# Optimization experiments

Measured on AMD Instinct MI355X. Metric: run time of the kernel, lower is better.

Reference implementation:

```python
import jax, jax.numpy as jnp
import numpy as np

B, S, D_MODEL, N_HEADS, D_FF = 4, 2048, 1024, 16, 4096
HEAD_DIM = D_MODEL // N_HEADS
NUM_BUCKETS, MAX_DISTANCE = 32, 128
EPS = 1e-6


def _relative_position_bucket(relative_position, num_buckets=NUM_BUCKETS, max_distance=MAX_DISTANCE):
    # bidirectional (encoder) variant, matching T5RelativePositionBias
    n = -relative_position
    nb = num_buckets // 2
    ret = (n < 0).astype(jnp.int32) * nb
    n = jnp.abs(n)
    max_exact = nb // 2
    val_if_large = max_exact + (
        jnp.log(jnp.maximum(n, 1).astype(jnp.float32) / max_exact)
        / np.log(max_distance / max_exact) * (nb - max_exact)
    ).astype(jnp.int32)
    val_if_large = jnp.minimum(val_if_large, nb - 1)
    return ret + jnp.where(n < max_exact, n, val_if_large)


def t5_position_bias(rel_emb, q_len, k_len):
    ctx = jnp.arange(q_len)[:, None]
    mem = jnp.arange(k_len)[None, :]
    rp_bucket = _relative_position_bucket(mem - ctx)          # [S, S]
    bias = rel_emb[rp_bucket]                                  # [S, S, H]
    return jnp.transpose(bias, (2, 0, 1))[None]                # [1, H, S, S]


def layer_norm(x, g, b):
    mu = jnp.mean(x, axis=-1, keepdims=True)
    var = jnp.mean(jnp.square(x - mu), axis=-1, keepdims=True)
    return (x - mu) * jax.lax.rsqrt(var + EPS) * g + b


def setup_inputs() -> dict:
    key = jax.random.key(0)
    ks = jax.random.split(key, 20)
    s = 0.02
    p = {
        'src': jax.random.normal(ks[0], (B, S, D_MODEL), jnp.float32),
        'wq': jax.random.normal(ks[1], (D_MODEL, D_MODEL), jnp.float32) * s,
        'bq': jnp.zeros((D_MODEL,), jnp.float32),
        'wk': jax.random.normal(ks[2], (D_MODEL, D_MODEL), jnp.float32) * s,
        'bk': jnp.zeros((D_MODEL,), jnp.float32),
        'wv': jax.random.normal(ks[3], (D_MODEL, D_MODEL), jnp.float32) * s,
        'bv': jnp.zeros((D_MODEL,), jnp.float32),
        'wo': jax.random.normal(ks[4], (D_MODEL, D_MODEL), jnp.float32) * s,
        'bo': jnp.zeros((D_MODEL,), jnp.float32),
        'w1': jax.random.normal(ks[5], (D_MODEL, D_FF), jnp.float32) * s,
        'b1': jnp.zeros((D_FF,), jnp.float32),
        'w2': jax.random.normal(ks[6], (D_FF, D_MODEL), jnp.float32) * s,
        'b2': jnp.zeros((D_MODEL,), jnp.float32),
        'ln1_g': jnp.ones((D_MODEL,), jnp.float32),
        'ln1_b': jnp.zeros((D_MODEL,), jnp.float32),
        'ln2_g': jnp.ones((D_MODEL,), jnp.float32),
        'ln2_b': jnp.zeros((D_MODEL,), jnp.float32),
        'rel_emb': jax.random.normal(ks[7], (NUM_BUCKETS, N_HEADS), jnp.float32) * s,
    }
    return p


def reference(src, wq, bq, wk, bk, wv, bv, wo, bo, w1, b1, w2, b2,
              ln1_g, ln1_b, ln2_g, ln2_b, rel_emb):
    b, s, _ = src.shape

    # --- self-attention block (pre-norm) ---
    xn = layer_norm(src, ln1_g, ln1_b)
    q = (xn @ wq + bq).reshape(b, s, N_HEADS, HEAD_DIM).transpose(0, 2, 1, 3)
    k = (xn @ wk + bk).reshape(b, s, N_HEADS, HEAD_DIM).transpose(0, 2, 1, 3)
    v = (xn @ wv + bv).reshape(b, s, N_HEADS, HEAD_DIM).transpose(0, 2, 1, 3)

    bias = t5_position_bias(rel_emb, s, s)                       # [1,H,S,S]
    scores = jnp.einsum('bhqd,bhkd->bhqk', q, k) / np.sqrt(HEAD_DIM) + bias
    attn = jax.nn.softmax(scores, axis=-1)
    ctx = jnp.einsum('bhqk,bhkd->bhqd', attn, v)                 # [B,H,S,Dh]
    ctx = ctx.transpose(0, 2, 1, 3).reshape(b, s, D_MODEL)
    x = src + (ctx @ wo + bo)

    # --- FFN block (pre-norm, ReLU) ---
    yn = layer_norm(x, ln2_g, ln2_b)
    y = jax.nn.relu(yn @ w1 + b1) @ w2 + b2
    return x + y
```

## Files before the change

kernel.cpp:

```cpp
#include <hip/hip_runtime.h>
#include <math.h>

typedef unsigned short u16;

#define S_LEN 2048
#define BSZ 4
#define DM 1024
#define NH 16
#define HD 64
#define DFF 4096
#define ROWS (BSZ * S_LEN)
#define LOG2E 1.4426950408889634f

typedef __attribute__((__ext_vector_type__(8))) __bf16 bf16x8;
typedef __attribute__((__ext_vector_type__(8))) short short8;
typedef __attribute__((__ext_vector_type__(4))) short short4v;
typedef __attribute__((__ext_vector_type__(4))) float f32x4;
typedef __attribute__((__ext_vector_type__(4))) float float4v;

__device__ __forceinline__ float bf2f(u16 u) {
    union { unsigned int i; float f; } c; c.i = ((unsigned int)u) << 16; return c.f;
}
__device__ __forceinline__ u16 f2bf(float f) {
    union { float f; unsigned int i; } c; c.f = f;
    unsigned int r = c.i + 0x7fffu + ((c.i >> 16) & 1u);
    return (u16)(r >> 16);
}
__device__ __forceinline__ u16 f2bf_cvt(float f) {
    __bf16 h = (__bf16)f;
    return __builtin_bit_cast(u16, h);
}
__device__ __forceinline__ float ldin(const void* p, long i, int f32) {
    return f32 ? ((const float*)p)[i] : bf2f(((const u16*)p)[i]);
}
__device__ __forceinline__ int dtype_f32(const u16* ln1g) {
    return ln1g[0] != 0x3F80;
}
__device__ __forceinline__ void gl_lds16(const void* g, void* l) {
    __builtin_amdgcn_global_load_lds(
        (const __attribute__((address_space(1))) unsigned int*)g,
        (__attribute__((address_space(3))) unsigned int*)l, 16, 0, 0);
}

#define BARR  asm volatile("s_barrier" ::: "memory")
#define LGKM0 asm volatile("s_waitcnt lgkmcnt(0)" ::: "memory")
#define VM4   asm volatile("s_waitcnt vmcnt(4)" ::: "memory")
#define VM2   asm volatile("s_waitcnt vmcnt(2)" ::: "memory")
#define VM0   asm volatile("s_waitcnt vmcnt(0)" ::: "memory")

__device__ __forceinline__ void tr_tile(
    const void* __restrict__ src, u16* __restrict__ dst, int N, int K,
    int bx, int by, int f32, int tid, u16 (*t)[72])
{
#pragma unroll
    for (int i = 0; i < 2; i++) {
        int c = tid + i * 256;
        int row = c >> 3, col = (c & 7) * 8;
        long off = (long)(by * 64 + row) * N + bx * 64 + col;
        short8 v;
        if (f32) {
            const float* s = (const float*)src + off;
            float4v a = *(const float4v*)s;
            float4v b = *(const float4v*)(s + 4);
#pragma unroll
            for (int k = 0; k < 4; k++) { v[k] = (short)f2bf(a[k]); v[k + 4] = (short)f2bf(b[k]); }
        } else {
            v = *(const short8*)((const u16*)src + off);
        }
        *(short8*)(&t[row][col]) = v;
    }
    __syncthreads();
#pragma unroll
    for (int i = 0; i < 2; i++) {
        int c = tid + i * 256;
        int row = c >> 3, col = (c & 7) * 8;
        short8 v;
#pragma unroll
        for (int jj = 0; jj < 8; jj++) v[jj] = (short)t[col + jj][row];
        *(short8*)(dst + (long)(bx * 64 + row) * K + by * 64 + col) = v;
    }
}

__global__ __launch_bounds__(256) void transpose4(
    const void* wq, const void* wk, const void* wv, const void* wo,
    u16* __restrict__ wqkvt, u16* __restrict__ wot, const u16* __restrict__ ln1g)
{
    __shared__ u16 t[64][72];
    int z = blockIdx.z;
    const void* src = (z == 0) ? wq : (z == 1) ? wk : (z == 2) ? wv : wo;
    u16* dst = (z < 3) ? wqkvt + (long)z * 1024 * 1024 : wot;
    tr_tile(src, dst, DM, DM, blockIdx.x, blockIdx.y, dtype_f32(ln1g), threadIdx.x, t);
}

__global__ __launch_bounds__(256) void transpose2(
    const void* w1, const void* w2, u16* __restrict__ w1t, u16* __restrict__ w2t,
    const u16* __restrict__ ln1g)
{
    __shared__ u16 t[64][72];
    int f32 = dtype_f32(ln1g);
    if (blockIdx.z == 0)
        tr_tile(w1, w1t, DFF, DM, blockIdx.x, blockIdx.y, f32, threadIdx.x, t);
    else
        tr_tile(w2, w2t, DM, DFF, blockIdx.y, blockIdx.x, f32, threadIdx.x, t);
}

__global__ __launch_bounds__(256) void vtrans(
    const u16* __restrict__ v, u16* __restrict__ vt)
{
    __shared__ u16 t[64][72];
    int s0 = blockIdx.x * 64;
    int bh = blockIdx.y;
    const u16* src = v + (long)bh * S_LEN * HD;
    u16* dst = vt + (long)bh * HD * S_LEN;
    int tid = threadIdx.x;
#pragma unroll
    for (int i = 0; i < 2; i++) {
        int c = tid + i * 256;
        int row = c >> 3, col = (c & 7) * 8;
        *(short8*)(&t[row][col]) = *(const short8*)(src + (long)(s0 + row) * HD + col);
    }
    __syncthreads();
#pragma unroll
    for (int i = 0; i < 2; i++) {
        int c = tid + i * 256;
        int row = c >> 3, col = (c & 7) * 8;
        short8 o;
#pragma unroll
        for (int jj = 0; jj < 8; jj++) o[jj] = (short)t[col + jj][row];
        *(short8*)(dst + (long)row * S_LEN + s0 + col) = o;
    }
}

__global__ __launch_bounds__(256) void prep_kernel(
    const void* bq, const void* bk, const void* bv, const void* bo,
    const void* b1, const void* b2, const void* l1g, const void* l1b,
    const void* l2g, const void* l2b, const void* rel,
    u16* __restrict__ smalls, float* __restrict__ bias_full)
{
    int f32 = dtype_f32((const u16*)l1g);
    int tid = blockIdx.x * blockDim.x + threadIdx.x;
    if (tid < 13312) {
        float v;
        if      (tid < 1024)  v = ldin(bq,  tid,         f32);
        else if (tid < 2048)  v = ldin(bk,  tid - 1024,  f32);
        else if (tid < 3072)  v = ldin(bv,  tid - 2048,  f32);
        else if (tid < 4096)  v = ldin(bo,  tid - 3072,  f32);
        else if (tid < 8192)  v = ldin(b1,  tid - 4096,  f32);
        else if (tid < 9216)  v = ldin(b2,  tid - 8192,  f32);
        else if (tid < 10240) v = ldin(l1g, tid - 9216,  f32);
        else if (tid < 11264) v = ldin(l1b, tid - 10240, f32);
        else if (tid < 12288) v = ldin(l2g, tid - 11264, f32);
        else                  v = ldin(l2b, tid - 12288, f32);
        smalls[tid] = f2bf(v);
    }
    if (tid < 4095 * 16) {
        int dIdx = tid >> 4;
        int h = tid & 15;
        int delta = dIdx - 2047;
        int n = -delta;
        int ret = (n < 0) ? 16 : 0;
        int na = (n < 0) ? -n : n;
        int bkt;
        if (na < 8) {
            bkt = na;
        } else {
            float tval = logf((float)na * 0.125f) * 2.8853900817779268f;
            int v = 8 + (int)tval;
            bkt = v < 15 ? v : 15;
        }
        bkt += ret;
        bias_full[h * 4095 + dIdx] = ldin(rel, bkt * 16 + h, f32) * LOG2E;
    }
}

__global__ __launch_bounds__(256) void ln_kernel(
    const void* __restrict__ xin, int external, const u16* __restrict__ ln1g,
    const u16* __restrict__ g, const u16* __restrict__ bta, u16* __restrict__ out)
{
    int f32 = external ? dtype_f32(ln1g) : 0;
    int row = blockIdx.x;
    int tid = threadIdx.x;
    float vals[4];
    if (f32) {
        float4v v = *(const float4v*)((const float*)xin + (long)row * DM + tid * 4);
#pragma unroll
        for (int k = 0; k < 4; k++) vals[k] = v[k];
    } else {
        short4v v = *(const short4v*)((const u16*)xin + (long)row * DM + tid * 4);
#pragma unroll
        for (int k = 0; k < 4; k++) vals[k] = bf2f((u16)v[k]);
    }
    float s1 = 0.f, s2 = 0.f;
#pragma unroll
    for (int k = 0; k < 4; k++) { s1 += vals[k]; s2 += vals[k] * vals[k]; }
#pragma unroll
    for (int off = 32; off > 0; off >>= 1) {
        s1 += __shfl_xor(s1, off);
        s2 += __shfl_xor(s2, off);
    }
    __shared__ float ps1[4], ps2[4];
    int wave = tid >> 6, lane = tid & 63;
    if (lane == 0) { ps1[wave] = s1; ps2[wave] = s2; }
    __syncthreads();
    s1 = ps1[0] + ps1[1] + ps1[2] + ps1[3];
    s2 = ps2[0] + ps2[1] + ps2[2] + ps2[3];
    float mu = s1 * (1.0f / DM);
    float var = s2 * (1.0f / DM) - mu * mu;
    float rs = rsqrtf(var + 1e-6f);
    short4v ov;
#pragma unroll
    for (int k = 0; k < 4; k++) {
        float gv = bf2f(g[tid * 4 + k]);
        float bv = bf2f(bta[tid * 4 + k]);
        ov[k] = (short)f2bf((vals[k] - mu) * rs * gv + bv);
    }
    *(short4v*)(out + (long)row * DM + tid * 4) = ov;
}

#define TM 256
#define TN 256
#define TK 64

#define PHASE(bi, q, STAGE, WAITV)                                             \
    {                                                                          \
        if ((q) == 0) {                                                        \
            _Pragma("unroll")                                                  \
            for (int j = 0; j < 4; j++) {                                      \
                _Pragma("unroll")                                              \
                for (int t = 0; t < 2; t++)                                    \
                    bfr[j][t] = __builtin_bit_cast(bf16x8, *(const short8*)(   \
                        &Bs[bi][wn * 64 + j * 16 + l16][((t * 4 + quad) ^ rxor) * 8])); \
            }                                                                  \
        }                                                                      \
        _Pragma("unroll")                                                      \
        for (int i = 0; i < 2; i++) {                                          \
            _Pragma("unroll")                                                  \
            for (int t = 0; t < 2; t++)                                        \
                af[i][t] = __builtin_bit_cast(bf16x8, *(const short8*)(        \
                    &As[bi][wm * 128 + ((q) * 2 + i) * 16 + l16][((t * 4 + quad) ^ rxor) * 8])); \
        }                                                                      \
        STAGE                                                                  \
        WAITV;                                                                 \
        BARR;                                                                  \
        LGKM0;                                                                 \
        __builtin_amdgcn_sched_barrier(0);                                     \
        __builtin_amdgcn_s_setprio(1);                                         \
        _Pragma("unroll")                                                      \
        for (int i = 0; i < 2; i++) {                                          \
            _Pragma("unroll")                                                  \
            for (int j = 0; j < 4; j++) {                                      \
                acc[(q) * 2 + i][j] = __builtin_amdgcn_mfma_f32_16x16x32_bf16( \
                    af[i][0], bfr[j][0], acc[(q) * 2 + i][j], 0, 0, 0);        \
                acc[(q) * 2 + i][j] = __builtin_amdgcn_mfma_f32_16x16x32_bf16( \
                    af[i][1], bfr[j][1], acc[(q) * 2 + i][j], 0, 0, 0);        \
            }                                                                  \
        }                                                                      \
        __builtin_amdgcn_s_setprio(0);                                         \
        BARR;                                                                  \
    }

__global__ __launch_bounds__(512, 2) void gemm256(
    const u16* __restrict__ A, const u16* __restrict__ Bt,
    const u16* __restrict__ bias, int M, int N, int K, int mode,
    u16* __restrict__ out_q, u16* __restrict__ out_k, u16* __restrict__ out_v,
    u16* __restrict__ outp)
{
    __shared__ u16 As[2][TM][TK];
    __shared__ u16 Bs[2][TN][TK];

    int tid = threadIdx.x;
    int wavei = tid >> 6, lane = tid & 63;
    int quad = lane >> 4, l16 = lane & 15;
    int wm = wavei >> 2, wn = wavei & 3;

    int nwg = gridDim.x * gridDim.y;
    int bid = blockIdx.y * gridDim.x + blockIdx.x;
    int chunk = nwg >> 3;
    int swz = (bid & 7) * chunk + (bid >> 3);
    int bx = swz % gridDim.x, by = swz / gridDim.x;
    long m0 = (long)by * TM, n0 = (long)bx * TN;

    int srow = tid >> 3;
    int pchk = tid & 7;
    int cchk = pchk ^ (srow & 7);
    int rxor = l16 & 7;

    int NT = K / TK;

    auto stageA = [&](int bufi, int h, int t) {
        const u16* g = A + (m0 + h * 128 + srow) * (long)K + (long)t * TK + cchk * 8;
        gl_lds16(g,                 &As[bufi][h * 128 + srow     ][pchk * 8]);
        gl_lds16(g + 64 * (long)K,  &As[bufi][h * 128 + srow + 64][pchk * 8]);
    };
    auto stageB = [&](int bufi, int h, int t) {
        const u16* g = Bt + (n0 + h * 128 + srow) * (long)K + (long)t * TK + cchk * 8;
        gl_lds16(g,                 &Bs[bufi][h * 128 + srow     ][pchk * 8]);
        gl_lds16(g + 64 * (long)K,  &Bs[bufi][h * 128 + srow + 64][pchk * 8]);
    };

    f32x4 acc[8][4];
    f32x4 z = {0.f, 0.f, 0.f, 0.f};
#pragma unroll
    for (int i = 0; i < 8; i++)
#pragma unroll
        for (int j = 0; j < 4; j++) acc[i][j] = z;

    bf16x8 bfr[4][2];
    bf16x8 af[2][2];

    stageA(0, 0, 0); stageA(0, 1, 0); stageB(0, 0, 0); stageB(0, 1, 0);
    stageB(1, 0, 1); stageB(1, 1, 1);
    VM4;
    BARR;

    for (int kt = 0; kt < NT - 2; kt += 2) {
        PHASE(0, 0, { stageA(1, 0, kt + 1); stageA(1, 1, kt + 1); }, (void)0);
        PHASE(0, 1, { stageB(0, 0, kt + 2); }, (void)0);
        PHASE(0, 2, { stageB(0, 1, kt + 2); }, (void)0);
        PHASE(0, 3, {}, VM4);
        PHASE(1, 0, { stageA(0, 0, kt + 2); }, (void)0);
        PHASE(1, 1, { stageA(0, 1, kt + 2); stageB(1, 0, kt + 3); }, (void)0);
        PHASE(1, 2, { stageB(1, 1, kt + 3); }, (void)0);
        PHASE(1, 3, {}, VM4);
    }
    PHASE(0, 0, { stageA(1, 0, NT - 1); stageA(1, 1, NT - 1); }, (void)0);
    PHASE(0, 1, {}, (void)0);
    PHASE(0, 2, {}, (void)0);
    PHASE(0, 3, {}, VM0);
    PHASE(1, 0, {}, (void)0);
    PHASE(1, 1, {}, (void)0);
    PHASE(1, 2, {}, (void)0);
    PHASE(1, 3, {}, (void)0);

#pragma unroll
    for (int i = 0; i < 8; i++) {
#pragma unroll
        for (int j = 0; j < 4; j++) {
#pragma unroll
            for (int r = 0; r < 4; r++) {
                long gr = m0 + wm * 128 + i * 16 + quad * 4 + r;
                long gc = n0 + wn * 64 + j * 16 + l16;
                float val = acc[i][j][r] + bf2f(bias[gc]);
                if (mode == 1) {
                    int sel = (int)(gc >> 10);
                    int cc = (int)(gc & 1023);
                    int h = cc >> 6, d = cc & 63;
                    int b = (int)(gr >> 11), s = (int)(gr & 2047);
                    u16* dst = (sel == 0) ? out_q : (sel == 1 ? out_k : out_v);
                    dst[(((long)(b * NH + h)) * S_LEN + s) * HD + d] = f2bf(val);
                } else {
                    outp[gr * (long)N + gc] = f2bf(val > 0.f ? val : 0.f);
                }
            }
        }
    }
}

#define NBM 256
#define NBN 128

#define PHN(bi, half, STAGE, WAITV)                                            \
    {                                                                          \
        if ((half) == 0) {                                                     \
            _Pragma("unroll")                                                  \
            for (int j = 0; j < 2; j++) {                                      \
                _Pragma("unroll")                                              \
                for (int t = 0; t < 2; t++)                                    \
                    nbfr[j][t] = __builtin_bit_cast(bf16x8, *(const short8*)(  \
                        &Bs[bi][wn * 32 + j * 16 + l16][((t * 4 + quad) ^ rxor) * 8])); \
            }                                                                  \
        }                                                                      \
        _Pragma("unroll")                                                      \
        for (int i = 0; i < 4; i++) {                                          \
            _Pragma("unroll")                                                  \
            for (int t = 0; t < 2; t++)                                        \
                naf[i][t] = __builtin_bit_cast(bf16x8, *(const short8*)(       \
                    &As[bi][wm * 128 + ((half) * 4 + i) * 16 + l16][((t * 4 + quad) ^ rxor) * 8])); \
        }                                                                      \
        STAGE                                                                  \
        WAITV;                                                                 \
        BARR;                                                                  \
        LGKM0;                                                                 \
        __builtin_amdgcn_sched_barrier(0);                                     \
        __builtin_amdgcn_s_setprio(1);                                         \
        _Pragma("unroll")                                                      \
        for (int i = 0; i < 4; i++) {                                          \
            _Pragma("unroll")                                                  \
            for (int j = 0; j < 2; j++) {                                      \
                acc[(half) * 4 + i][j] = __builtin_amdgcn_mfma_f32_16x16x32_bf16( \
                    naf[i][0], nbfr[j][0], acc[(half) * 4 + i][j], 0, 0, 0);   \
                acc[(half) * 4 + i][j] = __builtin_amdgcn_mfma_f32_16x16x32_bf16( \
                    naf[i][1], nbfr[j][1], acc[(half) * 4 + i][j], 0, 0, 0);   \
            }                                                                  \
        }                                                                      \
        __builtin_amdgcn_s_setprio(0);                                         \
        BARR;                                                                  \
    }

__global__ __launch_bounds__(512, 2) void gemm256n(
    const u16* __restrict__ A, const u16* __restrict__ Bt,
    const u16* __restrict__ bias, int M, int N, int K, int mode,
    const void* __restrict__ res, void* __restrict__ outp,
    const u16* __restrict__ ln1g)
{
    __shared__ u16 As[2][NBM][TK];
    __shared__ u16 Bs[2][NBN][TK];

    int tid = threadIdx.x;
    int wavei = tid >> 6, lane = tid & 63;
    int quad = lane >> 4, l16 = lane & 15;
    int wm = wavei >> 2, wn = wavei & 3;

    int nwg = gridDim.x * gridDim.y;
    int bid = blockIdx.y * gridDim.x + blockIdx.x;
    int chunk = nwg >> 3;
    int swz = (bid & 7) * chunk + (bid >> 3);
    int bx = swz % gridDim.x, by = swz / gridDim.x;
    long m0 = (long)by * NBM, n0 = (long)bx * NBN;
    int flg = dtype_f32(ln1g);

    int srow = tid >> 3;
    int pchk = tid & 7;
    int cchk = pchk ^ (srow & 7);
    int rxor = l16 & 7;

    int NT = K / TK;

    auto stageA = [&](int bufi, int h, int t) {
        const u16* g = A + (m0 + h * 128 + srow) * (long)K + (long)t * TK + cchk * 8;
        gl_lds16(g,                 &As[bufi][h * 128 + srow     ][pchk * 8]);
        gl_lds16(g + 64 * (long)K,  &As[bufi][h * 128 + srow + 64][pchk * 8]);
    };
    auto stageB = [&](int bufi, int t) {
        const u16* g = Bt + (n0 + srow) * (long)K + (long)t * TK + cchk * 8;
        gl_lds16(g,                 &Bs[bufi][srow     ][pchk * 8]);
        gl_lds16(g + 64 * (long)K,  &Bs[bufi][srow + 64][pchk * 8]);
    };

    f32x4 acc[8][2];
    f32x4 z = {0.f, 0.f, 0.f, 0.f};
#pragma unroll
    for (int i = 0; i < 8; i++)
#pragma unroll
        for (int j = 0; j < 2; j++) acc[i][j] = z;

    bf16x8 nbfr[2][2];
    bf16x8 naf[4][2];

    stageA(0, 0, 0); stageA(0, 1, 0); stageB(0, 0);
    stageB(1, 1);
    VM2;
    BARR;

    for (int kt = 0; kt < NT - 2; kt += 2) {
        PHN(0, 0, { stageA(1, 0, kt + 1); stageA(1, 1, kt + 1); }, (void)0);
        PHN(0, 1, { stageB(0, kt + 2); }, VM2);
        PHN(1, 0, { stageA(0, 0, kt + 2); stageA(0, 1, kt + 2); }, (void)0);
        PHN(1, 1, { stageB(1, kt + 3); }, VM2);
    }
    PHN(0, 0, { stageA(1, 0, NT - 1); stageA(1, 1, NT - 1); }, (void)0);
    PHN(0, 1, {}, VM0);
    PHN(1, 0, {}, (void)0);
    PHN(1, 1, {}, (void)0);

#pragma unroll
    for (int i = 0; i < 8; i++) {
#pragma unroll
        for (int j = 0; j < 2; j++) {
#pragma unroll
            for (int r = 0; r < 4; r++) {
                long gr = m0 + wm * 128 + i * 16 + quad * 4 + r;
                long gc = n0 + wn * 32 + j * 16 + l16;
                float val = acc[i][j][r] + bf2f(bias[gc]);
                long idx = gr * (long)N + gc;
                if (mode == 2) {
                    float rv = flg ? ((const float*)res)[idx]
                                   : bf2f(((const u16*)res)[idx]);
                    ((u16*)outp)[idx] = f2bf(val + rv);
                } else {
                    float o = val + bf2f(((const u16*)res)[idx]);
                    if (flg) ((float*)outp)[idx] = o;
                    else     ((u16*)outp)[idx]  = f2bf(o);
                }
            }
        }
    }
}

__global__ __launch_bounds__(512, 4) void attn_kernel(
    const u16* __restrict__ Qg, const u16* __restrict__ Kg, const u16* __restrict__ Vtg,
    const float* __restrict__ bias_full, u16* __restrict__ ctx)
{
    __shared__ u16 Ks[64][64];
    __shared__ u16 Vt[64][64];
    __shared__ u16 Ps[128][72];
    __shared__ u16 bias_s[2176];

    int bh = blockIdx.y;
    int b = bh >> 4, h = bh & 15;
    int q0 = blockIdx.x * 128;
    const u16* Q  = Qg  + (long)bh * S_LEN * HD;
    const u16* Kp = Kg  + (long)bh * S_LEN * HD;
    const u16* Vp = Vtg + (long)bh * HD * S_LEN;

    int tid = threadIdx.x;
    int wave = tid >> 6, lane = tid & 63;
    int quad = lane >> 4, l16 = lane & 15;

    for (int i = tid; i < 2176; i += 512)
        bias_s[i] = f2bf(bias_full[h * 4095 + 1920 + i - q0]);
    float Bneg = bias_full[h * 4095 + 0];
    float Bpos = bias_full[h * 4095 + 4094];

    int isv = wave >= 4;
    int t2 = tid & 255;
    int prow = t2 >> 3, pchk = t2 & 7;
    int cchk = pchk ^ (prow & 7);
    int rxor = l16 & 7;
    int rc0 = (quad ^ rxor) * 8;
    int rc1 = ((4 + quad) ^ rxor) * 8;

    bf16x8 aq[2];
#pragma unroll
    for (int t = 0; t < 2; t++)
        aq[t] = __builtin_bit_cast(bf16x8,
            *(const short8*)(Q + (long)(q0 + wave * 16 + l16) * HD + t * 32 + quad * 8));

    bf16x8 ones;
#pragma unroll
    for (int i = 0; i < 8; i++) ones[i] = (__bf16)1.0f;

    f32x4 o[4];
    f32x4 z = {0.f, 0.f, 0.f, 0.f};
#pragma unroll
    for (int j = 0; j < 4; j++) o[j] = z;
    f32x4 lacc = z;

    int ib = 127 + quad * 4 - wave * 16 - l16;
    const float c0 = 0.125f * LOG2E;

    auto compute = [&](int t0) {
        f32x4 s_[4];
#pragma unroll
        for (int j = 0; j < 4; j++) {
            f32x4 a = z;
            bf16x8 kf0 = __builtin_bit_cast(bf16x8, *(const short8*)(&Ks[j * 16 + l16][rc0]));
            a = __builtin_amdgcn_mfma_f32_16x16x32_bf16(kf0, aq[0], a, 0, 0, 0);
            bf16x8 kf1 = __builtin_bit_cast(bf16x8, *(const short8*)(&Ks[j * 16 + l16][rc1]));
            a = __builtin_amdgcn_mfma_f32_16x16x32_bf16(kf1, aq[1], a, 0, 0, 0);
            s_[j] = a;
        }
        int d0 = t0 - q0;
        int nearb = (d0 >= -153 && d0 <= 217);
        float bconst = (d0 > 0) ? Bpos : Bneg;
#pragma unroll
        for (int j = 0; j < 4; j++) {
            short4v pk;
#pragma unroll
            for (int r = 0; r < 4; r++) {
                float bl = nearb ? bf2f(bias_s[ib + t0 + j * 16 + r]) : bconst;
                float p = __builtin_amdgcn_exp2f(fmaf(s_[j][r], c0, bl));
                pk[r] = (short)f2bf_cvt(p);
            }
            *(short4v*)(&Ps[wave * 16 + l16][j * 16 + quad * 4]) = pk;
        }
        bf16x8 ap[2];
#pragma unroll
        for (int tt = 0; tt < 2; tt++)
            ap[tt] = __builtin_bit_cast(bf16x8,
                *(const short8*)(&Ps[wave * 16 + l16][tt * 32 + quad * 8]));
        lacc = __builtin_amdgcn_mfma_f32_16x16x32_bf16(ap[0], ones, lacc, 0, 0, 0);
        lacc = __builtin_amdgcn_mfma_f32_16x16x32_bf16(ap[1], ones, lacc, 0, 0, 0);
#pragma unroll
        for (int j = 0; j < 4; j++) {
            f32x4 t = o[j];
            bf16x8 bv0 = __builtin_bit_cast(bf16x8, *(const short8*)(&Vt[j * 16 + l16][rc0]));
            t = __builtin_amdgcn_mfma_f32_16x16x32_bf16(ap[0], bv0, t, 0, 0, 0);
            bf16x8 bv1 = __builtin_bit_cast(bf16x8, *(const short8*)(&Vt[j * 16 + l16][rc1]));
            t = __builtin_amdgcn_mfma_f32_16x16x32_bf16(ap[1], bv1, t, 0, 0, 0);
            o[j] = t;
        }
    };

    auto ld0 = [&](int t) -> short8 {
        return isv ? *(const short8*)(Vp + (long)prow * S_LEN + t + cchk * 8)
                   : *(const short8*)(Kp + (long)(t + prow) * HD + cchk * 8);
    };
    auto ld1 = [&](int t) -> short8 {
        return isv ? *(const short8*)(Vp + (long)(32 + prow) * S_LEN + t + cchk * 8)
                   : *(const short8*)(Kp + (long)(t + 32 + prow) * HD + cchk * 8);
    };
    u16* dst0 = isv ? &Vt[prow][pchk * 8] : &Ks[prow][pchk * 8];
    u16* dst1 = isv ? &Vt[32 + prow][pchk * 8] : &Ks[32 + prow][pchk * 8];

    short8 sa0 = ld0(0), sa1 = ld1(0);
    short8 sb0, sb1;

    for (int t0 = 0; t0 < S_LEN; t0 += 128) {
        if (t0 > 0) BARR;
        VM0;
        *(short8*)dst0 = sa0;
        *(short8*)dst1 = sa1;
        sb0 = ld0(t0 + 64);
        sb1 = ld1(t0 + 64);
        LGKM0; BARR;
        compute(t0);

        BARR;
        VM0;
        *(short8*)dst0 = sb0;
        *(short8*)dst1 = sb1;
        if (t0 + 128 < S_LEN) {
            sa0 = ld0(t0 + 128);
            sa1 = ld1(t0 + 128);
        }
        LGKM0; BARR;
        compute(t0 + 64);
    }

#pragma unroll
    for (int r = 0; r < 4; r++) {
        int qr = wave * 16 + quad * 4 + r;
        float linv = 1.0f / lacc[r];
        long srow2 = (long)(b * S_LEN + q0 + qr);
#pragma unroll
        for (int j = 0; j < 4; j++)
            ctx[srow2 * DM + h * HD + j * 16 + l16] = f2bf(o[j][r] * linv);
    }
}

extern "C" void kernel_launch(void* const* d_in, const int* in_sizes, int n_in,
                              void* d_out, int out_size, void* d_ws, size_t ws_size,
                              hipStream_t stream)
{
    const void* src  = d_in[0];
    const void* wq   = d_in[1];
    const void* bq   = d_in[2];
    const void* wk   = d_in[3];
    const void* bk   = d_in[4];
    const void* wv   = d_in[5];
    const void* bv   = d_in[6];
    const void* wo   = d_in[7];
    const void* bo   = d_in[8];
    const void* w1   = d_in[9];
    const void* b1   = d_in[10];
    const void* w2   = d_in[11];
    const void* b2   = d_in[12];
    const void* ln1g = d_in[13];
    const void* ln1b = d_in[14];
    const void* ln2g = d_in[15];
    const void* ln2b = d_in[16];
    const void* rel  = d_in[17];
    const u16* l1g16 = (const u16*)ln1g;

    char* ws = (char*)d_ws;
    const long MB = 1L << 20;
    u16*   smalls = (u16*)  (ws);
    float* bfull  = (float*)(ws + 65536);
    u16*   xn     = (u16*)  (ws + 1  * MB);
    u16*   vtg    = (u16*)  (ws + 1  * MB);
    u16*   qws    = (u16*)  (ws + 17 * MB);
    u16*   kws    = (u16*)  (ws + 33 * MB);
    u16*   vws    = (u16*)  (ws + 49 * MB);
    u16*   hbuf   = (u16*)  (ws + 1  * MB);
    u16*   ctx    = (u16*)  (ws + 65 * MB);
    u16*   yn     = (u16*)  (ws + 65 * MB);
    u16*   xbf    = (u16*)  (ws + 81 * MB);
    u16*   wqkvt  = (u16*)  (ws + 97 * MB);
    u16*   wot    = (u16*)  (ws + 103 * MB);
    u16*   w1t    = (u16*)  (ws + 97 * MB);
    u16*   w2t    = (u16*)  (ws + 105 * MB);

    transpose4<<<dim3(16, 16, 4), 256, 0, stream>>>(wq, wk, wv, wo, wqkvt, wot, l1g16);
    prep_kernel<<<256, 256, 0, stream>>>(bq, bk, bv, bo, b1, b2,
                                         ln1g, ln1b, ln2g, ln2b, rel,
                                         smalls, bfull);

    ln_kernel<<<ROWS, 256, 0, stream>>>(src, 1, l1g16,
                                        smalls + 9216, smalls + 10240, xn);

    gemm256<<<dim3(3072 / TN, ROWS / TM), 512, 0, stream>>>(
        xn, wqkvt, smalls + 0, ROWS, 3072, DM, 1, qws, kws, vws, nullptr);

    vtrans<<<dim3(S_LEN / 64, BSZ * NH), 256, 0, stream>>>(vws, vtg);

    attn_kernel<<<dim3(S_LEN / 128, BSZ * NH), 512, 0, stream>>>(qws, kws, vtg, bfull, ctx);

    gemm256n<<<dim3(DM / NBN, ROWS / NBM), 512, 0, stream>>>(
        ctx, wot, smalls + 3072, ROWS, DM, DM, 2, src, xbf, l1g16);

    transpose2<<<dim3(64, 16, 2), 256, 0, stream>>>(w1, w2, w1t, w2t, l1g16);

    ln_kernel<<<ROWS, 256, 0, stream>>>(xbf, 0, l1g16,
                                        smalls + 11264, smalls + 12288, yn);

    gemm256<<<dim3(DFF / TN, ROWS / TM), 512, 0, stream>>>(
        yn, w1t, smalls + 4096, ROWS, DFF, DM, 3, nullptr, nullptr, nullptr, hbuf);

    gemm256n<<<dim3(DM / NBN, ROWS / NBM), 512, 0, stream>>>(
        hbuf, w2t, smalls + 8192, ROWS, DM, DFF, 4, xbf, d_out, l1g16);
}
```

Measured before the change: 569.6 us.

## Merge weight transposes and prep into one launch; swizzle attention blocks

Combines the four-weight transpose, the FFN weight transpose and the bias/params prep into a single prep_all launch with a z-indexed grid, moving w1t/w2t to separate workspace regions so they are no longer overwritten. The attention kernel remaps block IDs with an XCD-style swizzle so consecutive blocks on one XCD share the same head's K/V in cache. It also pads the Ps shared tile row from 72 to 76 to change bank mapping. Launch count drops, but the merged grid has many early-exit idle blocks, and the padding change may alter LDS conflicts either way.

```diff
diff --git a/kernel.cpp b/kernel.cpp
--- a/kernel.cpp
+++ b/kernel.cpp
@@ -81,64 +81,38 @@
     }
 }
 
-__global__ __launch_bounds__(256) void transpose4(
+__global__ __launch_bounds__(256) void prep_all(
     const void* wq, const void* wk, const void* wv, const void* wo,
-    u16* __restrict__ wqkvt, u16* __restrict__ wot, const u16* __restrict__ ln1g)
+    const void* w1, const void* w2,
+    const void* bq, const void* bk, const void* bv, const void* bo,
+    const void* b1, const void* b2, const void* l1g, const void* l1b,
+    const void* l2g, const void* l2b, const void* rel,
+    u16* __restrict__ wqkvt, u16* __restrict__ wot,
+    u16* __restrict__ w1t, u16* __restrict__ w2t,
+    u16* __restrict__ smalls, float* __restrict__ bias_full)
 {
     __shared__ u16 t[64][72];
     int z = blockIdx.z;
-    const void* src = (z == 0) ? wq : (z == 1) ? wk : (z == 2) ? wv : wo;
-    u16* dst = (z < 3) ? wqkvt + (long)z * 1024 * 1024 : wot;
-    tr_tile(src, dst, DM, DM, blockIdx.x, blockIdx.y, dtype_f32(ln1g), threadIdx.x, t);
-}
-
-__global__ __launch_bounds__(256) void transpose2(
-    const void* w1, const void* w2, u16* __restrict__ w1t, u16* __restrict__ w2t,
-    const u16* __restrict__ ln1g)
-{
-    __shared__ u16 t[64][72];
-    int f32 = dtype_f32(ln1g);
-    if (blockIdx.z == 0)
+    int f32 = dtype_f32((const u16*)l1g);
+
+    if (z < 4) {
+        if (blockIdx.x >= 16) return;
+        const void* src = (z == 0) ? wq : (z == 1) ? wk : (z == 2) ? wv : wo;
+        u16* dst = (z < 3) ? wqkvt + (long)z * 1024 * 1024 : wot;
+        tr_tile(src, dst, DM, DM, blockIdx.x, blockIdx.y, f32, threadIdx.x, t);
+        return;
+    }
+    if (z == 4) {
         tr_tile(w1, w1t, DFF, DM, blockIdx.x, blockIdx.y, f32, threadIdx.x, t);
-    else
+        return;
+    }
+    if (z == 5) {
         tr_tile(w2, w2t, DM, DFF, blockIdx.y, blockIdx.x, f32, threadIdx.x, t);
-}
-
-__global__ __launch_bounds__(256) void vtrans(
-    const u16* __restrict__ v, u16* __restrict__ vt)
-{
-    __shared__ u16 t[64][72];
-    int s0 = blockIdx.x * 64;
-    int bh = blockIdx.y;
-    const u16* src = v + (long)bh * S_LEN * HD;
-    u16* dst = vt + (long)bh * HD * S_LEN;
-    int tid = threadIdx.x;
-#pragma unroll
-    for (int i = 0; i < 2; i++) {
-        int c = tid + i * 256;
-        int row = c >> 3, col = (c & 7) * 8;
-        *(short8*)(&t[row][col]) = *(const short8*)(src + (long)(s0 + row) * HD + col);
-    }
-    __syncthreads();
-#pragma unroll
-    for (int i = 0; i < 2; i++) {
-        int c = tid + i * 256;
-        int row = c >> 3, col = (c & 7) * 8;
-        short8 o;
-#pragma unroll
-        for (int jj = 0; jj < 8; jj++) o[jj] = (short)t[col + jj][row];
-        *(short8*)(dst + (long)row * S_LEN + s0 + col) = o;
-    }
-}
-
-__global__ __launch_bounds__(256) void prep_kernel(
-    const void* bq, const void* bk, const void* bv, const void* bo,
-    const void* b1, const void* b2, const void* l1g, const void* l1b,
-    const void* l2g, const void* l2b, const void* rel,
-    u16* __restrict__ smalls, float* __restrict__ bias_full)
-{
-    int f32 = dtype_f32((const u16*)l1g);
-    int tid = blockIdx.x * blockDim.x + threadIdx.x;
+        return;
+    }
+    int bidx = blockIdx.y * 64 + blockIdx.x;
+    if (bidx >= 256) return;
+    int tid = bidx * 256 + threadIdx.x;
     if (tid < 13312) {
         float v;
         if      (tid < 1024)  v = ldin(bq,  tid,         f32);
@@ -170,6 +144,33 @@
         }
         bkt += ret;
         bias_full[h * 4095 + dIdx] = ldin(rel, bkt * 16 + h, f32) * LOG2E;
+    }
+}
+
+__global__ __launch_bounds__(256) void vtrans(
+    const u16* __restrict__ v, u16* __restrict__ vt)
+{
+    __shared__ u16 t[64][72];
+    int s0 = blockIdx.x * 64;
+    int bh = blockIdx.y;
+    const u16* src = v + (long)bh * S_LEN * HD;
+    u16* dst = vt + (long)bh * HD * S_LEN;
+    int tid = threadIdx.x;
+#pragma unroll
+    for (int i = 0; i < 2; i++) {
+        int c = tid + i * 256;
+        int row = c >> 3, col = (c & 7) * 8;
+        *(short8*)(&t[row][col]) = *(const short8*)(src + (long)(s0 + row) * HD + col);
+    }
+    __syncthreads();
+#pragma unroll
+    for (int i = 0; i < 2; i++) {
+        int c = tid + i * 256;
+        int row = c >> 3, col = (c & 7) * 8;
+        short8 o;
+#pragma unroll
+        for (int jj = 0; jj < 8; jj++) o[jj] = (short)t[col + jj][row];
+        *(short8*)(dst + (long)row * S_LEN + s0 + col) = o;
     }
 }
 
@@ -493,12 +494,17 @@
 {
     __shared__ u16 Ks[64][64];
     __shared__ u16 Vt[64][64];
-    __shared__ u16 Ps[128][72];
+    __shared__ u16 Ps[128][76];
     __shared__ u16 bias_s[2176];
 
-    int bh = blockIdx.y;
+    int nwg = gridDim.x * gridDim.y;
+    int bid = blockIdx.y * gridDim.x + blockIdx.x;
+    int chunk = nwg >> 3;
+    int swz = (bid & 7) * chunk + (bid >> 3);
+    int qt = swz % gridDim.x, bh = swz / gridDim.x;
+
     int b = bh >> 4, h = bh & 15;
-    int q0 = blockIdx.x * 128;
+    int q0 = qt * 128;
     const u16* Q  = Qg  + (long)bh * S_LEN * HD;
     const u16* Kp = Kg  + (long)bh * S_LEN * HD;
     const u16* Vp = Vtg + (long)bh * HD * S_LEN;
@@ -668,13 +674,13 @@
     u16*   xbf    = (u16*)  (ws + 81 * MB);
     u16*   wqkvt  = (u16*)  (ws + 97 * MB);
     u16*   wot    = (u16*)  (ws + 103 * MB);
-    u16*   w1t    = (u16*)  (ws + 97 * MB);
-    u16*   w2t    = (u16*)  (ws + 105 * MB);
-
-    transpose4<<<dim3(16, 16, 4), 256, 0, stream>>>(wq, wk, wv, wo, wqkvt, wot, l1g16);
-    prep_kernel<<<256, 256, 0, stream>>>(bq, bk, bv, bo, b1, b2,
-                                         ln1g, ln1b, ln2g, ln2b, rel,
-                                         smalls, bfull);
+    u16*   w1t    = (u16*)  (ws + 105 * MB);
+    u16*   w2t    = (u16*)  (ws + 113 * MB);
+
+    prep_all<<<dim3(64, 16, 7), 256, 0, stream>>>(
+        wq, wk, wv, wo, w1, w2, bq, bk, bv, bo, b1, b2,
+        ln1g, ln1b, ln2g, ln2b, rel,
+        wqkvt, wot, w1t, w2t, smalls, bfull);
 
     ln_kernel<<<ROWS, 256, 0, stream>>>(src, 1, l1g16,
                                         smalls + 9216, smalls + 10240, xn);
@@ -689,8 +695,6 @@
     gemm256n<<<dim3(DM / NBN, ROWS / NBM), 512, 0, stream>>>(
         ctx, wot, smalls + 3072, ROWS, DM, DM, 2, src, xbf, l1g16);
 
-    transpose2<<<dim3(64, 16, 2), 256, 0, stream>>>(w1, w2, w1t, w2t, l1g16);
-
     ln_kernel<<<ROWS, 256, 0, stream>>>(xbf, 0, l1g16,
                                         smalls + 11264, smalls + 12288, yn);
 
```

Result: no change. 558.5 us (-1.9%).
